# Kernel optimization log

Measured on AMD Instinct MI355X. Metric: run time of the kernel, lower is better.

Reference implementation:

```python
import jax, jax.numpy as jnp
import numpy as np

STRIDE = 8  # window over x[:, max(0, i-stride) : i+1]


def setup_inputs() -> dict:
    key = jax.random.key(0)
    k0, k1, k2, k3, k4 = jax.random.split(key, 5)
    B, T, H = 16, 8192, 256
    x = jax.random.normal(k0, (B, T, H), dtype=jnp.float32)
    s = 1.0 / np.sqrt(H)  # torch nn.Linear default init range
    W_lin = jax.random.uniform(k1, (H, H), jnp.float32, -s, s)
    b_lin = jax.random.uniform(k2, (H,), jnp.float32, -s, s)
    W_mem = jax.random.uniform(k3, (H, H), jnp.float32, -s, s)
    b_mem = jax.random.uniform(k4, (H,), jnp.float32, -s, s)
    return {"x": x, "W_lin": W_lin, "b_lin": b_lin, "W_mem": W_mem, "b_mem": b_mem}


def reference(x, W_lin, b_lin, W_mem, b_mem):
    # x: [B, T, H]; input_dim == hidden_dim so input_lin is None in the original.
    B, T, H = x.shape
    # h = Linear(x)  (torch Linear: x @ W.T + b)
    h = jnp.einsum('bth,oh->bto', x, W_lin) + b_lin
    # Causal sliding-window mean over window [max(0, t-STRIDE), t] via cumsum.
    cs = jnp.cumsum(x, axis=1)                       # [B, T, H]
    idx = jnp.arange(T)
    start = jnp.maximum(0, idx - STRIDE)             # [T]
    prev = jnp.where((start > 0)[None, :, None],
                     cs[:, jnp.maximum(start - 1, 0)], 0.0)
    counts = (idx - start + 1).astype(x.dtype)       # min(t+1, STRIDE+1)
    means = (cs - prev) / counts[None, :, None]      # [B, T, H]
    # memory branch: Linear over window means, batched as one matmul
    mem = jnp.einsum('bth,oh->bto', means, W_mem) + b_mem
    return h + mem
```

## Files before the change

### kernel.cpp

```cpp
#include <hip/hip_runtime.h>
#include <hip/hip_bf16.h>

#define B_ 16
#define T_ 8192
#define H_ 256
#define M_ (B_ * T_)
#define K_ 512
#define STRIDE_ 8

typedef __bf16 bf16x8 __attribute__((ext_vector_type(8)));
typedef float f32x4 __attribute__((ext_vector_type(4)));

__device__ __forceinline__ unsigned short f2bf(float f) {
  unsigned u = __builtin_bit_cast(unsigned, f);
  u += 0x7fffu + ((u >> 16) & 1u);
  return (unsigned short)(u >> 16);
}

__device__ __forceinline__ void load_lds16(const void* g, void* l) {
  __builtin_amdgcn_global_load_lds(
      (const __attribute__((address_space(1))) void*)g,
      (__attribute__((address_space(3))) void*)l, 16, 0, 0);
}

__global__ __launch_bounds__(256) void wcat_kernel(
    const float* __restrict__ Wl, const float* __restrict__ bl,
    const float* __restrict__ Wm, const float* __restrict__ bm,
    unsigned short* __restrict__ Wcat, float* __restrict__ bias) {
  const int e = blockIdx.x * 256 + threadIdx.x;
  const int o = e >> 9;
  const int k = e & 511;
  const float w = (k < 256) ? Wl[o * 256 + k] : Wm[o * 256 + (k - 256)];
  Wcat[e] = f2bf(w);
  if (e < 256) bias[e] = bl[e] + bm[e];
}

__global__ __launch_bounds__(256) void prep_kernel(const float* __restrict__ x,
                                                   unsigned* __restrict__ Acat) {
  const int blk = blockIdx.x;
  const int b = blk >> 7;
  const int t0 = (blk & 127) << 6;
  const int g = threadIdx.x >> 7;
  const int p = threadIdx.x & 127;
  const int tbase = t0 + (g << 5);
  const float2* __restrict__ x2 = (const float2*)x;
  const size_t rb = (size_t)b * T_;

  float vx[40], vy[40];
#pragma unroll
  for (int i = 0; i < 40; ++i) {
    const int t = tbase - 8 + i;
    float xx = 0.f, yy = 0.f;
    if (t >= 0) {
      const float2 val = x2[(rb + t) * 128 + p];
      xx = val.x; yy = val.y;
    }
    vx[i] = xx; vy[i] = yy;
  }
  float sx = 0.f, sy = 0.f;
#pragma unroll
  for (int i = 0; i < 8; ++i) { sx += vx[i]; sy += vy[i]; }
#pragma unroll
  for (int r = 0; r < 32; ++r) {
    const int t = tbase + r;
    sx += vx[r + 8]; sy += vy[r + 8];
    const float cnt = (t >= STRIDE_) ? 9.f : (float)(t + 1);
    const float inv = __builtin_amdgcn_rcpf(cnt);
    const unsigned xpack =
        (unsigned)f2bf(vx[r + 8]) | ((unsigned)f2bf(vy[r + 8]) << 16);
    const unsigned mpack =
        (unsigned)f2bf(sx * inv) | ((unsigned)f2bf(sy * inv) << 16);
    const size_t row = rb + t;
    Acat[row * 256 + p] = xpack;
    Acat[row * 256 + 128 + p] = mpack;
    sx -= vx[r]; sy -= vy[r];
  }
}

__global__ __launch_bounds__(256) void gemm_kernel(
    const unsigned short* __restrict__ A,
    const unsigned short* __restrict__ Wc,
    const float* __restrict__ bias,
    float* __restrict__ out) {
  __shared__ __align__(16) unsigned short As[128 * 32];
  __shared__ __align__(16) unsigned short Bs[128 * 32];
  const int tid = threadIdx.x;
  const int m0 = blockIdx.x << 7;
  const int n0 = blockIdx.y << 7;
  const int w = tid >> 6;
  const int l = tid & 63;
  const int wr = (w >> 1) << 6;
  const int wc = (w & 1) << 6;
  const int lm = l & 15;
  const int kq = (l >> 4) << 3;

  const int f0 = tid, f1 = tid + 256;
  const size_t ga0 = (size_t)(m0 + (f0 >> 2)) * 512 + ((f0 & 3) << 3);
  const size_t ga1 = (size_t)(m0 + (f1 >> 2)) * 512 + ((f1 & 3) << 3);
  const size_t gb0 = (size_t)(n0 + (f0 >> 2)) * 512 + ((f0 & 3) << 3);
  const size_t gb1 = (size_t)(n0 + (f1 >> 2)) * 512 + ((f1 & 3) << 3);

  f32x4 acc[4][4];
#pragma unroll
  for (int i = 0; i < 4; ++i)
#pragma unroll
    for (int j = 0; j < 4; ++j) acc[i][j] = (f32x4){0.f, 0.f, 0.f, 0.f};

  for (int k0 = 0; k0 < K_; k0 += 32) {
    __syncthreads();
    load_lds16(A + ga0 + k0, &As[f0 * 8]);
    load_lds16(A + ga1 + k0, &As[f1 * 8]);
    load_lds16(Wc + gb0 + k0, &Bs[f0 * 8]);
    load_lds16(Wc + gb1 + k0, &Bs[f1 * 8]);
    __syncthreads();

    bf16x8 a[4], bb[4];
#pragma unroll
    for (int i = 0; i < 4; ++i)
      a[i] = *(const bf16x8*)&As[(wr + i * 16 + lm) * 32 + kq];
#pragma unroll
    for (int j = 0; j < 4; ++j)
      bb[j] = *(const bf16x8*)&Bs[(wc + j * 16 + lm) * 32 + kq];
#pragma unroll
    for (int i = 0; i < 4; ++i)
#pragma unroll
      for (int j = 0; j < 4; ++j)
        acc[i][j] =
            __builtin_amdgcn_mfma_f32_16x16x32_bf16(a[i], bb[j], acc[i][j], 0, 0, 0);
  }

  const int r0 = (l >> 4) << 2;
#pragma unroll
  for (int j = 0; j < 4; ++j) {
    const int o = n0 + wc + j * 16 + lm;
    const float bs = bias[o];
#pragma unroll
    for (int i = 0; i < 4; ++i) {
      const size_t mr = (size_t)(m0 + wr + i * 16 + r0);
#pragma unroll
      for (int r = 0; r < 4; ++r) out[(mr + r) * 256 + o] = acc[i][j][r] + bs;
    }
  }
}

extern "C" void kernel_launch(void* const* d_in, const int* in_sizes, int n_in,
                              void* d_out, int out_size, void* d_ws, size_t ws_size,
                              hipStream_t stream) {
  const float* x  = (const float*)d_in[0];
  const float* Wl = (const float*)d_in[1];
  const float* bl = (const float*)d_in[2];
  const float* Wm = (const float*)d_in[3];
  const float* bm = (const float*)d_in[4];
  float* out = (float*)d_out;

  char* ws = (char*)d_ws;
  unsigned* Acat = (unsigned*)ws;
  unsigned short* Wcat = (unsigned short*)(ws + (size_t)M_ * K_ * 2);
  float* bias = (float*)(ws + (size_t)M_ * K_ * 2 + (size_t)256 * 512 * 2);

  wcat_kernel<<<512, 256, 0, stream>>>(Wl, bl, Wm, bm, Wcat, bias);
  prep_kernel<<<2048, 256, 0, stream>>>(x, Acat);
  gemm_kernel<<<dim3(M_ / 128, 2), 256, 0, stream>>>(
      (const unsigned short*)Acat, Wcat, bias, out);
}
```

Before: 322.2 us.

## Fuse window-mean prep into GEMM, building bf16 A tiles in LDS from x

Removes the separate prep kernel and the 128 MiB bf16 Acat intermediate. The GEMM kernel now reads fp32 x directly, converts the first 8 K-chunks to bf16 and computes the sliding-window means for the last 8 K-chunks into LDS. This cuts global write and read traffic for the intermediate and one launch. In exchange, each block recomputes the window sums with 8-row halo reloads, both N-blocks redo the same prep, and the A loads become synchronous register loads instead of async LDS loads.

```diff
diff --git a/kernel.cpp b/kernel.cpp
--- a/kernel.cpp
+++ b/kernel.cpp
@@ -35,50 +35,8 @@
   if (e < 256) bias[e] = bl[e] + bm[e];
 }
 
-__global__ __launch_bounds__(256) void prep_kernel(const float* __restrict__ x,
-                                                   unsigned* __restrict__ Acat) {
-  const int blk = blockIdx.x;
-  const int b = blk >> 7;
-  const int t0 = (blk & 127) << 6;
-  const int g = threadIdx.x >> 7;
-  const int p = threadIdx.x & 127;
-  const int tbase = t0 + (g << 5);
-  const float2* __restrict__ x2 = (const float2*)x;
-  const size_t rb = (size_t)b * T_;
-
-  float vx[40], vy[40];
-#pragma unroll
-  for (int i = 0; i < 40; ++i) {
-    const int t = tbase - 8 + i;
-    float xx = 0.f, yy = 0.f;
-    if (t >= 0) {
-      const float2 val = x2[(rb + t) * 128 + p];
-      xx = val.x; yy = val.y;
-    }
-    vx[i] = xx; vy[i] = yy;
-  }
-  float sx = 0.f, sy = 0.f;
-#pragma unroll
-  for (int i = 0; i < 8; ++i) { sx += vx[i]; sy += vy[i]; }
-#pragma unroll
-  for (int r = 0; r < 32; ++r) {
-    const int t = tbase + r;
-    sx += vx[r + 8]; sy += vy[r + 8];
-    const float cnt = (t >= STRIDE_) ? 9.f : (float)(t + 1);
-    const float inv = __builtin_amdgcn_rcpf(cnt);
-    const unsigned xpack =
-        (unsigned)f2bf(vx[r + 8]) | ((unsigned)f2bf(vy[r + 8]) << 16);
-    const unsigned mpack =
-        (unsigned)f2bf(sx * inv) | ((unsigned)f2bf(sy * inv) << 16);
-    const size_t row = rb + t;
-    Acat[row * 256 + p] = xpack;
-    Acat[row * 256 + 128 + p] = mpack;
-    sx -= vx[r]; sy -= vy[r];
-  }
-}
-
-__global__ __launch_bounds__(256) void gemm_kernel(
-    const unsigned short* __restrict__ A,
+__global__ __launch_bounds__(256, 4) void fused_kernel(
+    const float* __restrict__ x,
     const unsigned short* __restrict__ Wc,
     const float* __restrict__ bias,
     float* __restrict__ out) {
@@ -87,6 +45,7 @@
   const int tid = threadIdx.x;
   const int m0 = blockIdx.x << 7;
   const int n0 = blockIdx.y << 7;
+  const int tb0 = m0 & (T_ - 1);
   const int w = tid >> 6;
   const int l = tid & 63;
   const int wr = (w >> 1) << 6;
@@ -95,10 +54,11 @@
   const int kq = (l >> 4) << 3;
 
   const int f0 = tid, f1 = tid + 256;
-  const size_t ga0 = (size_t)(m0 + (f0 >> 2)) * 512 + ((f0 & 3) << 3);
-  const size_t ga1 = (size_t)(m0 + (f1 >> 2)) * 512 + ((f1 & 3) << 3);
   const size_t gb0 = (size_t)(n0 + (f0 >> 2)) * 512 + ((f0 & 3) << 3);
   const size_t gb1 = (size_t)(n0 + (f1 >> 2)) * 512 + ((f1 & 3) << 3);
+
+  const int p_cp = tid & 15, p_g = tid >> 4;
+  const int q_c = tid & 31, q_g = tid >> 5;
 
   f32x4 acc[4][4];
 #pragma unroll
@@ -106,12 +66,44 @@
 #pragma unroll
     for (int j = 0; j < 4; ++j) acc[i][j] = (f32x4){0.f, 0.f, 0.f, 0.f};
 
-  for (int k0 = 0; k0 < K_; k0 += 32) {
+  for (int kc = 0; kc < 16; ++kc) {
     __syncthreads();
-    load_lds16(A + ga0 + k0, &As[f0 * 8]);
-    load_lds16(A + ga1 + k0, &As[f1 * 8]);
-    load_lds16(Wc + gb0 + k0, &Bs[f0 * 8]);
-    load_lds16(Wc + gb1 + k0, &Bs[f1 * 8]);
+    load_lds16(Wc + gb0 + kc * 32, &Bs[f0 * 8]);
+    load_lds16(Wc + gb1 + kc * 32, &Bs[f1 * 8]);
+
+    if (kc < 8) {
+      const int c = kc * 32;
+      const float2* __restrict__ x2 =
+          (const float2*)x + (size_t)(m0 + p_g * 8) * 128 + (c >> 1) + p_cp;
+      unsigned* __restrict__ As32 = (unsigned*)As;
+#pragma unroll
+      for (int r = 0; r < 8; ++r) {
+        const float2 v = x2[(size_t)r * 128];
+        As32[(p_g * 8 + r) * 16 + p_cp] =
+            (unsigned)f2bf(v.x) | ((unsigned)f2bf(v.y) << 16);
+      }
+    } else {
+      const int c = kc * 32 - 256;
+      float v[24];
+#pragma unroll
+      for (int i = 0; i < 24; ++i) {
+        const int lr = q_g * 16 - 8 + i;
+        const bool ok = (tb0 + lr) >= 0;
+        v[i] = ok ? x[(size_t)(m0 + lr) * 256 + c + q_c] : 0.f;
+      }
+      float s = 0.f;
+#pragma unroll
+      for (int i = 0; i < 8; ++i) s += v[i];
+#pragma unroll
+      for (int r = 0; r < 16; ++r) {
+        s += v[r + 8];
+        const int t = tb0 + q_g * 16 + r;
+        const float inv =
+            (t >= STRIDE_) ? (1.f / 9.f) : __builtin_amdgcn_rcpf((float)(t + 1));
+        As[(q_g * 16 + r) * 32 + q_c] = f2bf(s * inv);
+        s -= v[r];
+      }
+    }
     __syncthreads();
 
     bf16x8 a[4], bb[4];
@@ -154,12 +146,9 @@
   float* out = (float*)d_out;
 
   char* ws = (char*)d_ws;
-  unsigned* Acat = (unsigned*)ws;
-  unsigned short* Wcat = (unsigned short*)(ws + (size_t)M_ * K_ * 2);
-  float* bias = (float*)(ws + (size_t)M_ * K_ * 2 + (size_t)256 * 512 * 2);
+  unsigned short* Wcat = (unsigned short*)ws;
+  float* bias = (float*)(ws + (size_t)256 * 512 * 2);
 
   wcat_kernel<<<512, 256, 0, stream>>>(Wl, bl, Wm, bm, Wcat, bias);
-  prep_kernel<<<2048, 256, 0, stream>>>(x, Acat);
-  gemm_kernel<<<dim3(M_ / 128, 2), 256, 0, stream>>>(
-      (const unsigned short*)Acat, Wcat, bias, out);
+  fused_kernel<<<dim3(M_ / 128, 2), 256, 0, stream>>>(x, Wcat, bias, out);
 }
```

Result: slower. 332.6 us (+3.2%).
